# Kernel tuning notes

Measured on AMD Instinct MI355X. Metric: run time of the kernel, lower is better.

Reference implementation:

```python
import jax, jax.numpy as jnp
import numpy as np

N_FEATURES = 512
N_LAYERS = 128
BATCH = 2048
PI = np.pi


def setup_inputs() -> dict:
    key = jax.random.key(0)
    k0, k1, k2, k3, k4 = jax.random.split(key, 5)
    nA = N_FEATURES // 2            # angles per A layer (even pairs)
    nB = (N_FEATURES - 1) // 2      # angles per B layer (odd pairs)
    LB = N_LAYERS // 2
    LA = N_LAYERS - LB              # equal when N_LAYERS even
    return {
        "cmplx": jax.random.normal(k0, (BATCH, N_FEATURES, 2), dtype=jnp.float32),
        "angleA0": jax.random.uniform(k1, (LA, nA), jnp.float32, -PI, PI),
        "angleA1": jax.random.uniform(k2, (LA, nA), jnp.float32, -PI, PI),
        "angleB0": jax.random.uniform(k3, (LB, nB), jnp.float32, -PI, PI),
        "angleB1": jax.random.uniform(k4, (LB, nB), jnp.float32, -PI, PI),
        "omega": jnp.zeros((N_FEATURES,), jnp.float32),
    }


def _mzi(a, b, ang0, ang1):
    # MZI = DC . PS(ang1) . DC . PS(ang0) acting on mode pair (a, b)
    # U = 1/2 [[e^{i phi}(e^{i th}-1),    i(e^{i th}+1)   ],
    #          [i e^{i phi}(e^{i th}+1),  (1 - e^{i th})  ]]
    ephi = jnp.exp(1j * ang0)
    eth = jnp.exp(1j * ang1)
    t = 0.5 * (eth - 1.0)
    u = 0.5 * (eth + 1.0)
    na = ephi * t * a + 1j * u * b
    nb = 1j * ephi * u * a - t * b
    return na, nb


def _layer_A(x, a0, a1):
    # pairs (0,1),(2,3),...
    a = x[:, 0::2]
    b = x[:, 1::2]
    na, nb = _mzi(a, b, a0, a1)
    return jnp.stack([na, nb], axis=-1).reshape(x.shape)


def _layer_B(x, b0, b1):
    # pairs (1,2),(3,4),...; endpoints 0 and N-1 pass through (N even)
    N = x.shape[1]
    a = x[:, 1:N - 1:2]
    b = x[:, 2:N:2]
    na, nb = _mzi(a, b, b0, b1)
    mid = jnp.stack([na, nb], axis=-1).reshape(x.shape[0], N - 2)
    return jnp.concatenate([x[:, :1], mid, x[:, -1:]], axis=1)


def reference(cmplx, angleA0, angleA1, angleB0, angleB1, omega):
    x = cmplx[..., 0] + 1j * cmplx[..., 1]   # [B, N] complex64

    def step(x, angs):
        a0, a1, b0, b1 = angs
        x = _layer_A(x, a0, a1)
        x = _layer_B(x, b0, b1)
        return x, None

    x, _ = jax.lax.scan(step, x, (angleA0, angleA1, angleB0, angleB1))
    out = x * jnp.exp(1j * omega)            # complex diagonal phase
    return jnp.stack([out.real, out.imag], axis=-1)
```

## Files before the change

kernel.cpp:

```cpp
#include <hip/hip_runtime.h>

#define LSTEPS 64
#define NF 512
#define MB 2048
#define CSTRIDE 256
#define PL (NF * NF)
#define LDT 72

typedef __attribute__((ext_vector_type(8))) short bf16x8;
typedef __attribute__((ext_vector_type(4))) float f32x4;
typedef __attribute__((ext_vector_type(4))) int i32x4;

__device__ __forceinline__ float2 cmul(float2 a, float2 b) {
  return make_float2(fmaf(a.x, b.x, -(a.y * b.y)), fmaf(a.x, b.y, a.y * b.x));
}
__device__ __forceinline__ float2 cfma(float2 a, float2 b, float2 c) {
  return make_float2(fmaf(a.x, b.x, fmaf(-a.y, b.y, c.x)),
                     fmaf(a.x, b.y, fmaf(a.y, b.x, c.y)));
}
__device__ __forceinline__ unsigned short f2bf(float f) {
  union { float f; unsigned u; } v; v.f = f;
  unsigned r = v.u + 0x7FFF + ((v.u >> 16) & 1);
  return (unsigned short)(r >> 16);
}

__global__ __launch_bounds__(256) void prep_kernel(
    const float* __restrict__ a0, const float* __restrict__ a1,
    const float* __restrict__ b0, const float* __restrict__ b1,
    const float4* __restrict__ Xf,
    float4* __restrict__ cA, float4* __restrict__ cB,
    unsigned short* __restrict__ Xr, unsigned short* __restrict__ Xi)
{
  const int bid = blockIdx.x, tid = threadIdx.x;
  if (bid < 64) {
    const int l = bid;
    {
      float ang0 = a0[l * 256 + tid], ang1 = a1[l * 256 + tid];
      float se, ce, st, ct;
      sincosf(ang0, &se, &ce);
      sincosf(ang1, &st, &ct);
      float2 ephi = make_float2(ce, se);
      float2 tt = make_float2(0.5f * (ct - 1.0f), 0.5f * st);
      float2 uu = make_float2(0.5f * (ct + 1.0f), 0.5f * st);
      float2 C1 = cmul(ephi, tt);
      float2 C2 = make_float2(-uu.y, uu.x);
      float2 eu = cmul(ephi, uu);
      float2 C3 = make_float2(-eu.y, eu.x);
      float2 C4 = make_float2(-tt.x, -tt.y);
      float4* dst = cA + (size_t)(l * CSTRIDE + tid) * 2;
      dst[0] = make_float4(C1.x, C1.y, C2.x, C2.y);
      dst[1] = make_float4(C3.x, C3.y, C4.x, C4.y);
    }
    if (tid < 255) {
      float ang0 = b0[l * 255 + tid], ang1 = b1[l * 255 + tid];
      float se, ce, st, ct;
      sincosf(ang0, &se, &ce);
      sincosf(ang1, &st, &ct);
      float2 ephi = make_float2(ce, se);
      float2 tt = make_float2(0.5f * (ct - 1.0f), 0.5f * st);
      float2 uu = make_float2(0.5f * (ct + 1.0f), 0.5f * st);
      float2 C1 = cmul(ephi, tt);
      float2 C2 = make_float2(-uu.y, uu.x);
      float2 eu = cmul(ephi, uu);
      float2 C3 = make_float2(-eu.y, eu.x);
      float2 C4 = make_float2(-tt.x, -tt.y);
      float4* dst = cB + (size_t)(l * CSTRIDE + tid) * 2;
      dst[0] = make_float4(C1.x, C1.y, C2.x, C2.y);
      dst[1] = make_float4(C3.x, C3.y, C4.x, C4.y);
    } else {
      float4* dst = cB + (size_t)(l * CSTRIDE + 255) * 2;
      dst[0] = make_float4(0.f, 0.f, 0.f, 0.f);
      dst[1] = make_float4(0.f, 0.f, 0.f, 0.f);
    }
  } else {
    const int qi = (bid - 64) * 256 + tid;
    float4 v0 = Xf[(size_t)qi * 2];
    float4 v1 = Xf[(size_t)qi * 2 + 1];
    ushort4 r, im;
    r.x = f2bf(v0.x); im.x = f2bf(v0.y);
    r.y = f2bf(v0.z); im.y = f2bf(v0.w);
    r.z = f2bf(v1.x); im.z = f2bf(v1.y);
    r.w = f2bf(v1.z); im.w = f2bf(v1.w);
    *(ushort4*)(Xr + (size_t)qi * 4) = r;
    *(ushort4*)(Xi + (size_t)qi * 4) = im;
  }
}

struct MZS { float2 a0, b0, a1, b1; };

__device__ __forceinline__ void mzi_apply(const float4& k0, const float4& k1,
                                          float2& a, float2& b) {
  float2 c1 = make_float2(k0.x, k0.y), c2 = make_float2(k0.z, k0.w);
  float2 c3 = make_float2(k1.x, k1.y), c4 = make_float2(k1.z, k1.w);
  float2 na = cfma(c2, b, cmul(c1, a));
  float2 nb = cfma(c4, b, cmul(c3, a));
  a = na; b = nb;
}
__device__ __forceinline__ float2 mzi_bnd(const float4& k0, const float4& k1,
                                          float2& a, float2 b, bool en) {
  float2 d1 = make_float2(k0.x, k0.y), d2 = make_float2(k0.z, k0.w);
  float2 d3 = make_float2(k1.x, k1.y), d4 = make_float2(k1.z, k1.w);
  float2 na = cfma(d2, b, cmul(d1, a));
  float2 nb = cfma(d4, b, cmul(d3, a));
  if (en) a = na;
  return en ? nb : make_float2(0.f, 0.f);
}
__device__ __forceinline__ void load_bank(float4 (&K)[8],
    const float4* __restrict__ cA, const float4* __restrict__ cB, int l, int q0)
{
  const float4* pa = cA + (size_t)l * (CSTRIDE * 2) + (size_t)q0 * 2;
  const float4* pb = cB + (size_t)l * (CSTRIDE * 2) + (size_t)q0 * 2;
  K[0] = pa[0]; K[1] = pa[1]; K[2] = pa[2]; K[3] = pa[3];
  K[4] = pb[0]; K[5] = pb[1]; K[6] = pb[2]; K[7] = pb[3];
}
__device__ __forceinline__ void step_state(const float4 (&K)[8], int L, bool hasBnd,
                                           MZS& s)
{
  mzi_apply(K[0], K[1], s.a0, s.b0);
  mzi_apply(K[2], K[3], s.a1, s.b1);
  float xnx = __shfl_down(s.a0.x, 1);
  float xny = __shfl_down(s.a0.y, 1);
  float2 xn = (L == 63) ? make_float2(0.f, 0.f) : make_float2(xnx, xny);
  float2 nbo = mzi_bnd(K[6], K[7], s.b1, xn, hasBnd);
  mzi_apply(K[4], K[5], s.b0, s.a1);
  float px = __shfl_up(nbo.x, 1);
  float py = __shfl_up(nbo.y, 1);
  if (L > 0) s.a0 = make_float2(px, py);
}

__global__ __launch_bounds__(64) void chunk_mesh(
    const float4* __restrict__ cA, const float4* __restrict__ cB,
    unsigned short* __restrict__ Cb)
{
  const int bid = blockIdx.x;
  const int m = bid >> 8;
  const int cb = bid & 255;
  const int c = (cb & 7) * 32 + (cb >> 3);
  const int L = threadIdx.x;
  int ws = c - 63; ws = ws < 0 ? 0 : (ws > 128 ? 128 : ws);
  const int q0 = ws + 2 * L, q1 = q0 + 1;
  const bool hasBnd = (q1 < 255);

  MZS s0, s1;
  s0.a0 = make_float2((q0 == c) ? 1.f : 0.f, 0.f);
  s0.b0 = make_float2(0.f, 0.f);
  s0.a1 = make_float2((q1 == c) ? 1.f : 0.f, 0.f);
  s0.b1 = make_float2(0.f, 0.f);
  s1.a0 = make_float2(0.f, 0.f);
  s1.b0 = make_float2((q0 == c) ? 1.f : 0.f, 0.f);
  s1.a1 = make_float2(0.f, 0.f);
  s1.b1 = make_float2((q1 == c) ? 1.f : 0.f, 0.f);

  const int l0 = m * 16;
  float4 K0[8], K1[8];
  load_bank(K0, cA, cB, l0 + 0, q0);
  load_bank(K1, cA, cB, l0 + 1, q0);
#pragma unroll 1
  for (int i = 0; i < 14; i += 2) {
    step_state(K0, L, hasBnd, s0); step_state(K0, L, hasBnd, s1);
    load_bank(K0, cA, cB, l0 + ((i + 2 < 16) ? i + 2 : 15), q0);
    step_state(K1, L, hasBnd, s0); step_state(K1, L, hasBnd, s1);
    load_bank(K1, cA, cB, l0 + ((i + 3 < 16) ? i + 3 : 15), q0);
  }
  step_state(K0, L, hasBnd, s0); step_state(K0, L, hasBnd, s1);
  step_state(K1, L, hasBnd, s0); step_state(K1, L, hasBnd, s1);

  unsigned* nr32 = (unsigned*)(Cb + (size_t)m * 2 * PL);
  unsigned* ni32 = nr32 + PL / 2;
  const int rows[4] = {2 * q0, 2 * q0 + 1, 2 * q1, 2 * q1 + 1};
  const float2 v0[4] = {s0.a0, s0.b0, s0.a1, s0.b1};
  const float2 v1[4] = {s1.a0, s1.b0, s1.a1, s1.b1};
#pragma unroll
  for (int e = 0; e < 4; ++e) {
    unsigned pr = (unsigned)f2bf(v0[e].x) | ((unsigned)f2bf(v1[e].x) << 16);
    unsigned pi = (unsigned)f2bf(v0[e].y) | ((unsigned)f2bf(v1[e].y) << 16);
    nr32[(size_t)rows[e] * (NF / 2) + c] = pr;
    ni32[(size_t)rows[e] * (NF / 2) + c] = pi;
  }
#pragma unroll
  for (int e = 0; e < 4; ++e) {
    const int row = (2 * ws + 256 + 4 * L + e) & 511;
    nr32[(size_t)row * (NF / 2) + c] = 0u;
    ni32[(size_t)row * (NF / 2) + c] = 0u;
  }
}

template <bool FINAL>
__global__ __launch_bounds__(256) void gemm_kernel(
    const unsigned short* __restrict__ Zr, const unsigned short* __restrict__ Zi,
    const unsigned short* __restrict__ Cr, const unsigned short* __restrict__ Ci,
    unsigned short* __restrict__ Or, unsigned short* __restrict__ Oi,
    const float* __restrict__ omega, float2* __restrict__ Y)
{
  __shared__ __align__(16) unsigned short Ars[32][LDT];
  __shared__ __align__(16) unsigned short Ais[32][LDT];
  __shared__ __align__(16) unsigned short Brs[64][LDT];
  __shared__ __align__(16) unsigned short Bis[64][LDT];

  const int tid = threadIdx.x;
  const int w = tid >> 6, wm = w & 1, wn = w >> 1;
  const int lane = tid & 63;
  const int bm = (blockIdx.x >> 3) * 32;
  const int bn = (blockIdx.x & 7) * 64;

  int klo = bn - 40; if (klo < 0) klo = 0; klo &= ~63;
  int khi = bn + 104; if (khi > NF) khi = NF; khi = (khi + 63) & ~63;

  f32x4 acc_r[2], acc_i[2];
#pragma unroll
  for (int nf = 0; nf < 2; ++nf) {
    acc_r[nf] = (f32x4){0.f, 0.f, 0.f, 0.f};
    acc_i[nf] = (f32x4){0.f, 0.f, 0.f, 0.f};
  }
  const int sar = tid >> 3, sak = (tid & 7) * 8;
  const int sbr = tid >> 2, sbk = (tid & 3) * 16;

  for (int k0 = klo; k0 < khi; k0 += 64) {
    const uint4* gar = (const uint4*)(Zr + (size_t)(bm + sar) * NF + k0 + sak);
    const uint4* gai = (const uint4*)(Zi + (size_t)(bm + sar) * NF + k0 + sak);
    const uint4* gbr = (const uint4*)(Cr + (size_t)(bn + sbr) * NF + k0 + sbk);
    const uint4* gbi = (const uint4*)(Ci + (size_t)(bn + sbr) * NF + k0 + sbk);
    uint4 ar = gar[0];
    uint4 ai = gai[0];
    uint4 br0 = gbr[0], br1 = gbr[1];
    uint4 bi0 = gbi[0], bi1 = gbi[1];

    if (k0 > klo) __syncthreads();

    *(uint4*)&Ars[sar][sak]     = ar;
    *(uint4*)&Ais[sar][sak]     = ai;
    *(uint4*)&Brs[sbr][sbk]     = br0;
    *(uint4*)&Brs[sbr][sbk + 8] = br1;
    *(uint4*)&Bis[sbr][sbk]     = bi0;
    *(uint4*)&Bis[sbr][sbk + 8] = bi1;

    __syncthreads();

#pragma unroll
    for (int kk = 0; kk < 2; ++kk) {
      const int ko = kk * 32 + (lane >> 4) * 8;
      bf16x8 afr = *(const bf16x8*)&Ars[wm * 16 + (lane & 15)][ko];
      bf16x8 afi = *(const bf16x8*)&Ais[wm * 16 + (lane & 15)][ko];
      i32x4 neg = (i32x4)afi ^ (int)0x80008000;
      bf16x8 afin = (bf16x8)neg;
#pragma unroll
      for (int nf = 0; nf < 2; ++nf) {
        bf16x8 bfr = *(const bf16x8*)&Brs[wn * 32 + nf * 16 + (lane & 15)][ko];
        bf16x8 bfi = *(const bf16x8*)&Bis[wn * 32 + nf * 16 + (lane & 15)][ko];
        acc_r[nf] = __builtin_amdgcn_mfma_f32_16x16x32_bf16(afr,  bfr, acc_r[nf], 0, 0, 0);
        acc_r[nf] = __builtin_amdgcn_mfma_f32_16x16x32_bf16(afin, bfi, acc_r[nf], 0, 0, 0);
        acc_i[nf] = __builtin_amdgcn_mfma_f32_16x16x32_bf16(afr,  bfi, acc_i[nf], 0, 0, 0);
        acc_i[nf] = __builtin_amdgcn_mfma_f32_16x16x32_bf16(afi,  bfr, acc_i[nf], 0, 0, 0);
      }
    }
  }

  const int dn0 = bn + wn * 32 + (lane & 15);
  const int dm0 = bm + wm * 16 + (lane >> 4) * 4;
#pragma unroll
  for (int nf = 0; nf < 2; ++nf) {
    const int n = dn0 + nf * 16;
    if (FINAL) {
      float sn, cn;
      sincosf(omega[n], &sn, &cn);
#pragma unroll
      for (int r = 0; r < 4; ++r) {
        float yr = acc_r[nf][r], yi = acc_i[nf][r];
        Y[(size_t)(dm0 + r) * NF + n] =
            make_float2(fmaf(yr, cn, -(yi * sn)), fmaf(yr, sn, yi * cn));
      }
    } else {
#pragma unroll
      for (int r = 0; r < 4; ++r) {
        Or[(size_t)(dm0 + r) * NF + n] = f2bf(acc_r[nf][r]);
        Oi[(size_t)(dm0 + r) * NF + n] = f2bf(acc_i[nf][r]);
      }
    }
  }
}

extern "C" void kernel_launch(void* const* d_in, const int* in_sizes, int n_in,
                              void* d_out, int out_size, void* d_ws, size_t ws_size,
                              hipStream_t stream) {
  const float* cmplx = (const float*)d_in[0];
  const float* a0    = (const float*)d_in[1];
  const float* a1    = (const float*)d_in[2];
  const float* b0    = (const float*)d_in[3];
  const float* b1    = (const float*)d_in[4];
  const float* omega = (const float*)d_in[5];

  size_t off = 0;
  float4* cA = (float4*)((char*)d_ws + off); off += (size_t)LSTEPS * CSTRIDE * 2 * sizeof(float4);
  float4* cB = (float4*)((char*)d_ws + off); off += (size_t)LSTEPS * CSTRIDE * 2 * sizeof(float4);
  unsigned short* Xr = (unsigned short*)((char*)d_ws + off); off += (size_t)MB * NF * 2;
  unsigned short* Xi = (unsigned short*)((char*)d_ws + off); off += (size_t)MB * NF * 2;
  unsigned short* Cb = (unsigned short*)((char*)d_ws + off); off += (size_t)4 * 2 * PL * 2;
  unsigned short* Z1r = (unsigned short*)((char*)d_ws + off); off += (size_t)MB * NF * 2;
  unsigned short* Z1i = (unsigned short*)((char*)d_ws + off); off += (size_t)MB * NF * 2;
  unsigned short* Z2r = (unsigned short*)((char*)d_ws + off); off += (size_t)MB * NF * 2;
  unsigned short* Z2i = (unsigned short*)((char*)d_ws + off); off += (size_t)MB * NF * 2;
  float2* Y = (float2*)d_out;

  prep_kernel<<<1088, 256, 0, stream>>>(a0, a1, b0, b1, (const float4*)cmplx,
                                        cA, cB, Xr, Xi);
  chunk_mesh<<<1024, 64, 0, stream>>>(cA, cB, Cb);

  const unsigned short* C0r = Cb;               const unsigned short* C0i = Cb + PL;
  const unsigned short* C1r = Cb + 2 * PL;      const unsigned short* C1i = Cb + 3 * PL;
  const unsigned short* C2r = Cb + 4 * PL;      const unsigned short* C2i = Cb + 5 * PL;
  const unsigned short* C3r = Cb + 6 * PL;      const unsigned short* C3i = Cb + 7 * PL;

  const int grid = (MB / 32) * (NF / 64);
  gemm_kernel<false><<<grid, 256, 0, stream>>>(Xr,  Xi,  C0r, C0i, Z1r, Z1i, omega, Y);
  gemm_kernel<false><<<grid, 256, 0, stream>>>(Z1r, Z1i, C1r, C1i, Z2r, Z2i, omega, Y);
  gemm_kernel<false><<<grid, 256, 0, stream>>>(Z2r, Z2i, C2r, C2i, Z1r, Z1i, omega, Y);
  gemm_kernel<true> <<<grid, 256, 0, stream>>>(Z1r, Z1i, C3r, C3i, Z2r, Z2i, omega, Y);
}
```

Baseline: 51.08 us.

## Split mesh into two 32-step chunks instead of four 16-step chunks

The layer stack is now composed into two banded transfer matrices of 32 steps each instead of four of 16 steps. Each chunk_mesh block traces four basis states (two columns) over 32 steps, so there are fewer blocks and each does more serial work. The downstream pass drops from four banded complex GEMMs to two, with a wider K band (bandwidth grows with chunk depth). The intent is fewer launches and less Z round-tripping through memory, at the cost of a longer serial chunk_mesh critical path and more MACs per GEMM.

```diff
diff --git a/kernel.cpp b/kernel.cpp
--- a/kernel.cpp
+++ b/kernel.cpp
@@ -127,61 +127,99 @@
   float py = __shfl_up(nbo.y, 1);
   if (L > 0) s.a0 = make_float2(px, py);
 }
+__device__ __forceinline__ void step4(const float4 (&K)[8], int L, bool hasBnd,
+                                      MZS& s0, MZS& s1, MZS& s2, MZS& s3)
+{
+  step_state(K, L, hasBnd, s0);
+  step_state(K, L, hasBnd, s1);
+  step_state(K, L, hasBnd, s2);
+  step_state(K, L, hasBnd, s3);
+}
 
 __global__ __launch_bounds__(64) void chunk_mesh(
     const float4* __restrict__ cA, const float4* __restrict__ cB,
     unsigned short* __restrict__ Cb)
 {
   const int bid = blockIdx.x;
-  const int m = bid >> 8;
-  const int cb = bid & 255;
-  const int c = (cb & 7) * 32 + (cb >> 3);
+  const int m = bid >> 7;
+  const int gb = bid & 127;
+  const int g = (gb & 7) * 16 + (gb >> 3);
   const int L = threadIdx.x;
-  int ws = c - 63; ws = ws < 0 ? 0 : (ws > 128 ? 128 : ws);
+  int ws = 2 * g - 62; ws = ws < 0 ? 0 : (ws > 128 ? 128 : ws);
   const int q0 = ws + 2 * L, q1 = q0 + 1;
   const bool hasBnd = (q1 < 255);
-
-  MZS s0, s1;
-  s0.a0 = make_float2((q0 == c) ? 1.f : 0.f, 0.f);
+  const int p0 = 2 * g, p1 = 2 * g + 1;
+
+  MZS s0, s1, s2, s3;
+  s0.a0 = make_float2((q0 == p0) ? 1.f : 0.f, 0.f);
   s0.b0 = make_float2(0.f, 0.f);
-  s0.a1 = make_float2((q1 == c) ? 1.f : 0.f, 0.f);
+  s0.a1 = make_float2((q1 == p0) ? 1.f : 0.f, 0.f);
   s0.b1 = make_float2(0.f, 0.f);
   s1.a0 = make_float2(0.f, 0.f);
-  s1.b0 = make_float2((q0 == c) ? 1.f : 0.f, 0.f);
+  s1.b0 = make_float2((q0 == p0) ? 1.f : 0.f, 0.f);
   s1.a1 = make_float2(0.f, 0.f);
-  s1.b1 = make_float2((q1 == c) ? 1.f : 0.f, 0.f);
-
-  const int l0 = m * 16;
+  s1.b1 = make_float2((q1 == p0) ? 1.f : 0.f, 0.f);
+  s2.a0 = make_float2((q0 == p1) ? 1.f : 0.f, 0.f);
+  s2.b0 = make_float2(0.f, 0.f);
+  s2.a1 = make_float2((q1 == p1) ? 1.f : 0.f, 0.f);
+  s2.b1 = make_float2(0.f, 0.f);
+  s3.a0 = make_float2(0.f, 0.f);
+  s3.b0 = make_float2((q0 == p1) ? 1.f : 0.f, 0.f);
+  s3.a1 = make_float2(0.f, 0.f);
+  s3.b1 = make_float2((q1 == p1) ? 1.f : 0.f, 0.f);
+
+  const int l0 = m * 32;
   float4 K0[8], K1[8];
   load_bank(K0, cA, cB, l0 + 0, q0);
   load_bank(K1, cA, cB, l0 + 1, q0);
 #pragma unroll 1
-  for (int i = 0; i < 14; i += 2) {
-    step_state(K0, L, hasBnd, s0); step_state(K0, L, hasBnd, s1);
-    load_bank(K0, cA, cB, l0 + ((i + 2 < 16) ? i + 2 : 15), q0);
-    step_state(K1, L, hasBnd, s0); step_state(K1, L, hasBnd, s1);
-    load_bank(K1, cA, cB, l0 + ((i + 3 < 16) ? i + 3 : 15), q0);
-  }
-  step_state(K0, L, hasBnd, s0); step_state(K0, L, hasBnd, s1);
-  step_state(K1, L, hasBnd, s0); step_state(K1, L, hasBnd, s1);
+  for (int i = 0; i < 30; i += 2) {
+    step4(K0, L, hasBnd, s0, s1, s2, s3);
+    load_bank(K0, cA, cB, l0 + i + 2, q0);
+    step4(K1, L, hasBnd, s0, s1, s2, s3);
+    load_bank(K1, cA, cB, l0 + i + 3, q0);
+  }
+  step4(K0, L, hasBnd, s0, s1, s2, s3);
+  step4(K1, L, hasBnd, s0, s1, s2, s3);
 
   unsigned* nr32 = (unsigned*)(Cb + (size_t)m * 2 * PL);
   unsigned* ni32 = nr32 + PL / 2;
   const int rows[4] = {2 * q0, 2 * q0 + 1, 2 * q1, 2 * q1 + 1};
-  const float2 v0[4] = {s0.a0, s0.b0, s0.a1, s0.b1};
-  const float2 v1[4] = {s1.a0, s1.b0, s1.a1, s1.b1};
-#pragma unroll
-  for (int e = 0; e < 4; ++e) {
-    unsigned pr = (unsigned)f2bf(v0[e].x) | ((unsigned)f2bf(v1[e].x) << 16);
-    unsigned pi = (unsigned)f2bf(v0[e].y) | ((unsigned)f2bf(v1[e].y) << 16);
-    nr32[(size_t)rows[e] * (NF / 2) + c] = pr;
-    ni32[(size_t)rows[e] * (NF / 2) + c] = pi;
-  }
-#pragma unroll
-  for (int e = 0; e < 4; ++e) {
-    const int row = (2 * ws + 256 + 4 * L + e) & 511;
-    nr32[(size_t)row * (NF / 2) + c] = 0u;
-    ni32[(size_t)row * (NF / 2) + c] = 0u;
+  {
+    const int cc = 2 * g;
+    const float2 v0[4] = {s0.a0, s0.b0, s0.a1, s0.b1};
+    const float2 v1[4] = {s1.a0, s1.b0, s1.a1, s1.b1};
+#pragma unroll
+    for (int e = 0; e < 4; ++e) {
+      unsigned pr = (unsigned)f2bf(v0[e].x) | ((unsigned)f2bf(v1[e].x) << 16);
+      unsigned pi = (unsigned)f2bf(v0[e].y) | ((unsigned)f2bf(v1[e].y) << 16);
+      nr32[(size_t)rows[e] * (NF / 2) + cc] = pr;
+      ni32[(size_t)rows[e] * (NF / 2) + cc] = pi;
+    }
+#pragma unroll
+    for (int e = 0; e < 4; ++e) {
+      const int row = (2 * ws + 256 + 4 * L + e) & 511;
+      nr32[(size_t)row * (NF / 2) + cc] = 0u;
+      ni32[(size_t)row * (NF / 2) + cc] = 0u;
+    }
+  }
+  {
+    const int cc = 2 * g + 1;
+    const float2 v0[4] = {s2.a0, s2.b0, s2.a1, s2.b1};
+    const float2 v1[4] = {s3.a0, s3.b0, s3.a1, s3.b1};
+#pragma unroll
+    for (int e = 0; e < 4; ++e) {
+      unsigned pr = (unsigned)f2bf(v0[e].x) | ((unsigned)f2bf(v1[e].x) << 16);
+      unsigned pi = (unsigned)f2bf(v0[e].y) | ((unsigned)f2bf(v1[e].y) << 16);
+      nr32[(size_t)rows[e] * (NF / 2) + cc] = pr;
+      ni32[(size_t)rows[e] * (NF / 2) + cc] = pi;
+    }
+#pragma unroll
+    for (int e = 0; e < 4; ++e) {
+      const int row = (2 * ws + 256 + 4 * L + e) & 511;
+      nr32[(size_t)row * (NF / 2) + cc] = 0u;
+      ni32[(size_t)row * (NF / 2) + cc] = 0u;
+    }
   }
 }
 
@@ -203,8 +241,8 @@
   const int bm = (blockIdx.x >> 3) * 32;
   const int bn = (blockIdx.x & 7) * 64;
 
-  int klo = bn - 40; if (klo < 0) klo = 0; klo &= ~63;
-  int khi = bn + 104; if (khi > NF) khi = NF; khi = (khi + 63) & ~63;
+  int klo = bn - 72; if (klo < 0) klo = 0; klo &= ~63;
+  int khi = bn + 136; if (khi > NF) khi = NF; khi = (khi + 63) & ~63;
 
   f32x4 acc_r[2], acc_i[2];
 #pragma unroll
@@ -294,25 +332,19 @@
   float4* cB = (float4*)((char*)d_ws + off); off += (size_t)LSTEPS * CSTRIDE * 2 * sizeof(float4);
   unsigned short* Xr = (unsigned short*)((char*)d_ws + off); off += (size_t)MB * NF * 2;
   unsigned short* Xi = (unsigned short*)((char*)d_ws + off); off += (size_t)MB * NF * 2;
-  unsigned short* Cb = (unsigned short*)((char*)d_ws + off); off += (size_t)4 * 2 * PL * 2;
+  unsigned short* Cb = (unsigned short*)((char*)d_ws + off); off += (size_t)2 * 2 * PL * 2;
   unsigned short* Z1r = (unsigned short*)((char*)d_ws + off); off += (size_t)MB * NF * 2;
   unsigned short* Z1i = (unsigned short*)((char*)d_ws + off); off += (size_t)MB * NF * 2;
-  unsigned short* Z2r = (unsigned short*)((char*)d_ws + off); off += (size_t)MB * NF * 2;
-  unsigned short* Z2i = (unsigned short*)((char*)d_ws + off); off += (size_t)MB * NF * 2;
   float2* Y = (float2*)d_out;
 
   prep_kernel<<<1088, 256, 0, stream>>>(a0, a1, b0, b1, (const float4*)cmplx,
                                         cA, cB, Xr, Xi);
-  chunk_mesh<<<1024, 64, 0, stream>>>(cA, cB, Cb);
+  chunk_mesh<<<256, 64, 0, stream>>>(cA, cB, Cb);
 
   const unsigned short* C0r = Cb;               const unsigned short* C0i = Cb + PL;
   const unsigned short* C1r = Cb + 2 * PL;      const unsigned short* C1i = Cb + 3 * PL;
-  const unsigned short* C2r = Cb + 4 * PL;      const unsigned short* C2i = Cb + 5 * PL;
-  const unsigned short* C3r = Cb + 6 * PL;      const unsigned short* C3i = Cb + 7 * PL;
 
   const int grid = (MB / 32) * (NF / 64);
   gemm_kernel<false><<<grid, 256, 0, stream>>>(Xr,  Xi,  C0r, C0i, Z1r, Z1i, omega, Y);
-  gemm_kernel<false><<<grid, 256, 0, stream>>>(Z1r, Z1i, C1r, C1i, Z2r, Z2i, omega, Y);
-  gemm_kernel<false><<<grid, 256, 0, stream>>>(Z2r, Z2i, C2r, C2i, Z1r, Z1i, omega, Y);
-  gemm_kernel<true> <<<grid, 256, 0, stream>>>(Z1r, Z1i, C3r, C3i, Z2r, Z2i, omega, Y);
-}
+  gemm_kernel<true> <<<grid, 256, 0, stream>>>(Z1r, Z1i, C1r, C1i, nullptr, nullptr, omega, Y);
+}
```

After: 54.47 us. 1.07x slower.

## Split mesh into two 32-layer chunks and fuse input conversion into first GEMM

Applied to the files above, without the earlier changes.

Replaces four 16-layer banded transfer matrices with two 32-layer ones, so only two banded complex GEMMs run instead of four, each with a wider K band. The chunk_mesh kernel now propagates one basis column per block (1024 blocks, 32 layer steps each) instead of two columns per block over 16 steps. The fp32-to-bf16 split of the input moves from the prep kernel into the first GEMM's A-tile load, removing a separate pass and intermediate buffers. The trade-off is a wider K band per GEMM, longer serial chains in chunk_mesh, and narrower A-tile stores and converts inside the GEMM loop.

```diff
diff --git a/kernel.cpp b/kernel.cpp
--- a/kernel.cpp
+++ b/kernel.cpp
@@ -1,6 +1,5 @@
 #include <hip/hip_runtime.h>
 
-#define LSTEPS 64
 #define NF 512
 #define MB 2048
 #define CSTRIDE 256
@@ -27,62 +26,46 @@
 __global__ __launch_bounds__(256) void prep_kernel(
     const float* __restrict__ a0, const float* __restrict__ a1,
     const float* __restrict__ b0, const float* __restrict__ b1,
-    const float4* __restrict__ Xf,
-    float4* __restrict__ cA, float4* __restrict__ cB,
-    unsigned short* __restrict__ Xr, unsigned short* __restrict__ Xi)
-{
-  const int bid = blockIdx.x, tid = threadIdx.x;
-  if (bid < 64) {
-    const int l = bid;
-    {
-      float ang0 = a0[l * 256 + tid], ang1 = a1[l * 256 + tid];
-      float se, ce, st, ct;
-      sincosf(ang0, &se, &ce);
-      sincosf(ang1, &st, &ct);
-      float2 ephi = make_float2(ce, se);
-      float2 tt = make_float2(0.5f * (ct - 1.0f), 0.5f * st);
-      float2 uu = make_float2(0.5f * (ct + 1.0f), 0.5f * st);
-      float2 C1 = cmul(ephi, tt);
-      float2 C2 = make_float2(-uu.y, uu.x);
-      float2 eu = cmul(ephi, uu);
-      float2 C3 = make_float2(-eu.y, eu.x);
-      float2 C4 = make_float2(-tt.x, -tt.y);
-      float4* dst = cA + (size_t)(l * CSTRIDE + tid) * 2;
-      dst[0] = make_float4(C1.x, C1.y, C2.x, C2.y);
-      dst[1] = make_float4(C3.x, C3.y, C4.x, C4.y);
-    }
-    if (tid < 255) {
-      float ang0 = b0[l * 255 + tid], ang1 = b1[l * 255 + tid];
-      float se, ce, st, ct;
-      sincosf(ang0, &se, &ce);
-      sincosf(ang1, &st, &ct);
-      float2 ephi = make_float2(ce, se);
-      float2 tt = make_float2(0.5f * (ct - 1.0f), 0.5f * st);
-      float2 uu = make_float2(0.5f * (ct + 1.0f), 0.5f * st);
-      float2 C1 = cmul(ephi, tt);
-      float2 C2 = make_float2(-uu.y, uu.x);
-      float2 eu = cmul(ephi, uu);
-      float2 C3 = make_float2(-eu.y, eu.x);
-      float2 C4 = make_float2(-tt.x, -tt.y);
-      float4* dst = cB + (size_t)(l * CSTRIDE + tid) * 2;
-      dst[0] = make_float4(C1.x, C1.y, C2.x, C2.y);
-      dst[1] = make_float4(C3.x, C3.y, C4.x, C4.y);
-    } else {
-      float4* dst = cB + (size_t)(l * CSTRIDE + 255) * 2;
-      dst[0] = make_float4(0.f, 0.f, 0.f, 0.f);
-      dst[1] = make_float4(0.f, 0.f, 0.f, 0.f);
-    }
+    float4* __restrict__ cA, float4* __restrict__ cB)
+{
+  const int l = blockIdx.x, tid = threadIdx.x;
+  {
+    float ang0 = a0[l * 256 + tid], ang1 = a1[l * 256 + tid];
+    float se, ce, st, ct;
+    sincosf(ang0, &se, &ce);
+    sincosf(ang1, &st, &ct);
+    float2 ephi = make_float2(ce, se);
+    float2 tt = make_float2(0.5f * (ct - 1.0f), 0.5f * st);
+    float2 uu = make_float2(0.5f * (ct + 1.0f), 0.5f * st);
+    float2 C1 = cmul(ephi, tt);
+    float2 C2 = make_float2(-uu.y, uu.x);
+    float2 eu = cmul(ephi, uu);
+    float2 C3 = make_float2(-eu.y, eu.x);
+    float2 C4 = make_float2(-tt.x, -tt.y);
+    float4* dst = cA + (size_t)(l * CSTRIDE + tid) * 2;
+    dst[0] = make_float4(C1.x, C1.y, C2.x, C2.y);
+    dst[1] = make_float4(C3.x, C3.y, C4.x, C4.y);
+  }
+  if (tid < 255) {
+    float ang0 = b0[l * 255 + tid], ang1 = b1[l * 255 + tid];
+    float se, ce, st, ct;
+    sincosf(ang0, &se, &ce);
+    sincosf(ang1, &st, &ct);
+    float2 ephi = make_float2(ce, se);
+    float2 tt = make_float2(0.5f * (ct - 1.0f), 0.5f * st);
+    float2 uu = make_float2(0.5f * (ct + 1.0f), 0.5f * st);
+    float2 C1 = cmul(ephi, tt);
+    float2 C2 = make_float2(-uu.y, uu.x);
+    float2 eu = cmul(ephi, uu);
+    float2 C3 = make_float2(-eu.y, eu.x);
+    float2 C4 = make_float2(-tt.x, -tt.y);
+    float4* dst = cB + (size_t)(l * CSTRIDE + tid) * 2;
+    dst[0] = make_float4(C1.x, C1.y, C2.x, C2.y);
+    dst[1] = make_float4(C3.x, C3.y, C4.x, C4.y);
   } else {
-    const int qi = (bid - 64) * 256 + tid;
-    float4 v0 = Xf[(size_t)qi * 2];
-    float4 v1 = Xf[(size_t)qi * 2 + 1];
-    ushort4 r, im;
-    r.x = f2bf(v0.x); im.x = f2bf(v0.y);
-    r.y = f2bf(v0.z); im.y = f2bf(v0.w);
-    r.z = f2bf(v1.x); im.z = f2bf(v1.y);
-    r.w = f2bf(v1.z); im.w = f2bf(v1.w);
-    *(ushort4*)(Xr + (size_t)qi * 4) = r;
-    *(ushort4*)(Xi + (size_t)qi * 4) = im;
+    float4* dst = cB + (size_t)(l * CSTRIDE + 255) * 2;
+    dst[0] = make_float4(0.f, 0.f, 0.f, 0.f);
+    dst[1] = make_float4(0.f, 0.f, 0.f, 0.f);
   }
 }
 
@@ -133,60 +116,59 @@
     unsigned short* __restrict__ Cb)
 {
   const int bid = blockIdx.x;
-  const int m = bid >> 8;
-  const int cb = bid & 255;
-  const int c = (cb & 7) * 32 + (cb >> 3);
+  const int m = bid >> 9;
+  const int cb = bid & 511;
+  const int j = (cb & 7) * 64 + (cb >> 3);
   const int L = threadIdx.x;
-  int ws = c - 63; ws = ws < 0 ? 0 : (ws > 128 ? 128 : ws);
+  const int p0 = j >> 1;
+  int ws = p0 - 63; ws = ws < 0 ? 0 : (ws > 128 ? 128 : ws);
   const int q0 = ws + 2 * L, q1 = q0 + 1;
   const bool hasBnd = (q1 < 255);
 
-  MZS s0, s1;
-  s0.a0 = make_float2((q0 == c) ? 1.f : 0.f, 0.f);
-  s0.b0 = make_float2(0.f, 0.f);
-  s0.a1 = make_float2((q1 == c) ? 1.f : 0.f, 0.f);
-  s0.b1 = make_float2(0.f, 0.f);
-  s1.a0 = make_float2(0.f, 0.f);
-  s1.b0 = make_float2((q0 == c) ? 1.f : 0.f, 0.f);
-  s1.a1 = make_float2(0.f, 0.f);
-  s1.b1 = make_float2((q1 == c) ? 1.f : 0.f, 0.f);
-
-  const int l0 = m * 16;
-  float4 K0[8], K1[8];
+  MZS s;
+  s.a0 = make_float2((2 * q0     == j) ? 1.f : 0.f, 0.f);
+  s.b0 = make_float2((2 * q0 + 1 == j) ? 1.f : 0.f, 0.f);
+  s.a1 = make_float2((2 * q1     == j) ? 1.f : 0.f, 0.f);
+  s.b1 = make_float2((2 * q1 + 1 == j) ? 1.f : 0.f, 0.f);
+
+  const int l0 = m * 32;
+  float4 K0[8], K1[8], K2[8];
   load_bank(K0, cA, cB, l0 + 0, q0);
   load_bank(K1, cA, cB, l0 + 1, q0);
+  load_bank(K2, cA, cB, l0 + 2, q0);
+
 #pragma unroll 1
-  for (int i = 0; i < 14; i += 2) {
-    step_state(K0, L, hasBnd, s0); step_state(K0, L, hasBnd, s1);
-    load_bank(K0, cA, cB, l0 + ((i + 2 < 16) ? i + 2 : 15), q0);
-    step_state(K1, L, hasBnd, s0); step_state(K1, L, hasBnd, s1);
-    load_bank(K1, cA, cB, l0 + ((i + 3 < 16) ? i + 3 : 15), q0);
-  }
-  step_state(K0, L, hasBnd, s0); step_state(K0, L, hasBnd, s1);
-  step_state(K1, L, hasBnd, s0); step_state(K1, L, hasBnd, s1);
-
-  unsigned* nr32 = (unsigned*)(Cb + (size_t)m * 2 * PL);
-  unsigned* ni32 = nr32 + PL / 2;
+  for (int i = 0; i < 30; i += 3) {
+    step_state(K0, L, hasBnd, s);
+    load_bank(K0, cA, cB, l0 + ((i + 3 < 32) ? i + 3 : 31), q0);
+    step_state(K1, L, hasBnd, s);
+    load_bank(K1, cA, cB, l0 + ((i + 4 < 32) ? i + 4 : 31), q0);
+    step_state(K2, L, hasBnd, s);
+    load_bank(K2, cA, cB, l0 + ((i + 5 < 32) ? i + 5 : 31), q0);
+  }
+  step_state(K0, L, hasBnd, s);
+  step_state(K1, L, hasBnd, s);
+
+  unsigned short* Cr = Cb + (size_t)m * 2 * PL;
+  unsigned short* Ci = Cr + PL;
   const int rows[4] = {2 * q0, 2 * q0 + 1, 2 * q1, 2 * q1 + 1};
-  const float2 v0[4] = {s0.a0, s0.b0, s0.a1, s0.b1};
-  const float2 v1[4] = {s1.a0, s1.b0, s1.a1, s1.b1};
+  const float2 vals[4] = {s.a0, s.b0, s.a1, s.b1};
 #pragma unroll
   for (int e = 0; e < 4; ++e) {
-    unsigned pr = (unsigned)f2bf(v0[e].x) | ((unsigned)f2bf(v1[e].x) << 16);
-    unsigned pi = (unsigned)f2bf(v0[e].y) | ((unsigned)f2bf(v1[e].y) << 16);
-    nr32[(size_t)rows[e] * (NF / 2) + c] = pr;
-    ni32[(size_t)rows[e] * (NF / 2) + c] = pi;
+    Cr[(size_t)rows[e] * NF + j] = f2bf(vals[e].x);
+    Ci[(size_t)rows[e] * NF + j] = f2bf(vals[e].y);
   }
 #pragma unroll
   for (int e = 0; e < 4; ++e) {
     const int row = (2 * ws + 256 + 4 * L + e) & 511;
-    nr32[(size_t)row * (NF / 2) + c] = 0u;
-    ni32[(size_t)row * (NF / 2) + c] = 0u;
-  }
-}
-
-template <bool FINAL>
+    Cr[(size_t)row * NF + j] = 0;
+    Ci[(size_t)row * NF + j] = 0;
+  }
+}
+
+template <int MODE>
 __global__ __launch_bounds__(256) void gemm_kernel(
+    const float2* __restrict__ Xf,
     const unsigned short* __restrict__ Zr, const unsigned short* __restrict__ Zi,
     const unsigned short* __restrict__ Cr, const unsigned short* __restrict__ Ci,
     unsigned short* __restrict__ Or, unsigned short* __restrict__ Oi,
@@ -203,8 +185,8 @@
   const int bm = (blockIdx.x >> 3) * 32;
   const int bn = (blockIdx.x & 7) * 64;
 
-  int klo = bn - 40; if (klo < 0) klo = 0; klo &= ~63;
-  int khi = bn + 104; if (khi > NF) khi = NF; khi = (khi + 63) & ~63;
+  int klo = bn - 72; if (klo < 0) klo = 0; klo &= ~63;
+  int khi = bn + 136; if (khi > NF) khi = NF; khi = (khi + 63) & ~63;
 
   f32x4 acc_r[2], acc_i[2];
 #pragma unroll
@@ -216,23 +198,38 @@
   const int sbr = tid >> 2, sbk = (tid & 3) * 16;
 
   for (int k0 = klo; k0 < khi; k0 += 64) {
-    const uint4* gar = (const uint4*)(Zr + (size_t)(bm + sar) * NF + k0 + sak);
-    const uint4* gai = (const uint4*)(Zi + (size_t)(bm + sar) * NF + k0 + sak);
+    ushort4 ar2[2], ai2[2];
+    if (MODE == 0) {
+      const float4* xs = (const float4*)(Xf + (size_t)(bm + sar) * NF + k0 + sak);
+#pragma unroll
+      for (int h = 0; h < 2; ++h) {
+        float4 v0 = xs[2 * h], v1 = xs[2 * h + 1];
+        ar2[h].x = f2bf(v0.x); ai2[h].x = f2bf(v0.y);
+        ar2[h].y = f2bf(v0.z); ai2[h].y = f2bf(v0.w);
+        ar2[h].z = f2bf(v1.x); ai2[h].z = f2bf(v1.y);
+        ar2[h].w = f2bf(v1.z); ai2[h].w = f2bf(v1.w);
+      }
+    } else {
+      const ushort4* gr = (const ushort4*)(Zr + (size_t)(bm + sar) * NF + k0 + sak);
+      const ushort4* gi = (const ushort4*)(Zi + (size_t)(bm + sar) * NF + k0 + sak);
+      ar2[0] = gr[0]; ar2[1] = gr[1];
+      ai2[0] = gi[0]; ai2[1] = gi[1];
+    }
     const uint4* gbr = (const uint4*)(Cr + (size_t)(bn + sbr) * NF + k0 + sbk);
     const uint4* gbi = (const uint4*)(Ci + (size_t)(bn + sbr) * NF + k0 + sbk);
-    uint4 ar = gar[0];
-    uint4 ai = gai[0];
     uint4 br0 = gbr[0], br1 = gbr[1];
     uint4 bi0 = gbi[0], bi1 = gbi[1];
 
     if (k0 > klo) __syncthreads();
 
-    *(uint4*)&Ars[sar][sak]     = ar;
-    *(uint4*)&Ais[sar][sak]     = ai;
-    *(uint4*)&Brs[sbr][sbk]     = br0;
-    *(uint4*)&Brs[sbr][sbk + 8] = br1;
-    *(uint4*)&Bis[sbr][sbk]     = bi0;
-    *(uint4*)&Bis[sbr][sbk + 8] = bi1;
+    *(ushort4*)&Ars[sar][sak]     = ar2[0];
+    *(ushort4*)&Ars[sar][sak + 4] = ar2[1];
+    *(ushort4*)&Ais[sar][sak]     = ai2[0];
+    *(ushort4*)&Ais[sar][sak + 4] = ai2[1];
+    *(uint4*)&Brs[sbr][sbk]       = br0;
+    *(uint4*)&Brs[sbr][sbk + 8]   = br1;
+    *(uint4*)&Bis[sbr][sbk]       = bi0;
+    *(uint4*)&Bis[sbr][sbk + 8]   = bi1;
 
     __syncthreads();
 
@@ -260,7 +257,7 @@
 #pragma unroll
   for (int nf = 0; nf < 2; ++nf) {
     const int n = dn0 + nf * 16;
-    if (FINAL) {
+    if (MODE == 1) {
       float sn, cn;
       sincosf(omega[n], &sn, &cn);
 #pragma unroll
@@ -282,7 +279,7 @@
 extern "C" void kernel_launch(void* const* d_in, const int* in_sizes, int n_in,
                               void* d_out, int out_size, void* d_ws, size_t ws_size,
                               hipStream_t stream) {
-  const float* cmplx = (const float*)d_in[0];
+  const float2* Xf   = (const float2*)d_in[0];
   const float* a0    = (const float*)d_in[1];
   const float* a1    = (const float*)d_in[2];
   const float* b0    = (const float*)d_in[3];
@@ -290,29 +287,22 @@
   const float* omega = (const float*)d_in[5];
 
   size_t off = 0;
-  float4* cA = (float4*)((char*)d_ws + off); off += (size_t)LSTEPS * CSTRIDE * 2 * sizeof(float4);
-  float4* cB = (float4*)((char*)d_ws + off); off += (size_t)LSTEPS * CSTRIDE * 2 * sizeof(float4);
-  unsigned short* Xr = (unsigned short*)((char*)d_ws + off); off += (size_t)MB * NF * 2;
-  unsigned short* Xi = (unsigned short*)((char*)d_ws + off); off += (size_t)MB * NF * 2;
-  unsigned short* Cb = (unsigned short*)((char*)d_ws + off); off += (size_t)4 * 2 * PL * 2;
+  float4* cA = (float4*)((char*)d_ws + off); off += (size_t)64 * CSTRIDE * 2 * sizeof(float4);
+  float4* cB = (float4*)((char*)d_ws + off); off += (size_t)64 * CSTRIDE * 2 * sizeof(float4);
+  unsigned short* Cb  = (unsigned short*)((char*)d_ws + off); off += (size_t)2 * 2 * PL * 2;
   unsigned short* Z1r = (unsigned short*)((char*)d_ws + off); off += (size_t)MB * NF * 2;
   unsigned short* Z1i = (unsigned short*)((char*)d_ws + off); off += (size_t)MB * NF * 2;
-  unsigned short* Z2r = (unsigned short*)((char*)d_ws + off); off += (size_t)MB * NF * 2;
-  unsigned short* Z2i = (unsigned short*)((char*)d_ws + off); off += (size_t)MB * NF * 2;
   float2* Y = (float2*)d_out;
 
-  prep_kernel<<<1088, 256, 0, stream>>>(a0, a1, b0, b1, (const float4*)cmplx,
-                                        cA, cB, Xr, Xi);
+  const unsigned short* C0r = Cb;           const unsigned short* C0i = Cb + PL;
+  const unsigned short* C1r = Cb + 2 * PL;  const unsigned short* C1i = Cb + 3 * PL;
+
+  prep_kernel<<<64, 256, 0, stream>>>(a0, a1, b0, b1, cA, cB);
   chunk_mesh<<<1024, 64, 0, stream>>>(cA, cB, Cb);
 
-  const unsigned short* C0r = Cb;               const unsigned short* C0i = Cb + PL;
-  const unsigned short* C1r = Cb + 2 * PL;      const unsigned short* C1i = Cb + 3 * PL;
-  const unsigned short* C2r = Cb + 4 * PL;      const unsigned short* C2i = Cb + 5 * PL;
-  const unsigned short* C3r = Cb + 6 * PL;      const unsigned short* C3i = Cb + 7 * PL;
-
   const int grid = (MB / 32) * (NF / 64);
-  gemm_kernel<false><<<grid, 256, 0, stream>>>(Xr,  Xi,  C0r, C0i, Z1r, Z1i, omega, Y);
-  gemm_kernel<false><<<grid, 256, 0, stream>>>(Z1r, Z1i, C1r, C1i, Z2r, Z2i, omega, Y);
-  gemm_kernel<false><<<grid, 256, 0, stream>>>(Z2r, Z2i, C2r, C2i, Z1r, Z1i, omega, Y);
-  gemm_kernel<true> <<<grid, 256, 0, stream>>>(Z1r, Z1i, C3r, C3i, Z2r, Z2i, omega, Y);
-}
+  gemm_kernel<0><<<grid, 256, 0, stream>>>(Xf, nullptr, nullptr, C0r, C0i,
+                                           Z1r, Z1i, omega, Y);
+  gemm_kernel<1><<<grid, 256, 0, stream>>>(nullptr, Z1r, Z1i, C1r, C1i,
+                                           nullptr, nullptr, omega, Y);
+}
```

Result: faster. 49.02 us (-4.0%).
